# Kernel tuning notes

Hardware: AMD Instinct MI355X
Metric: run time of the kernel (lower is better)

The kernel has to match this reference:

```python
import jax, jax.numpy as jnp
import numpy as np

NEG_INF = -9e15  # same masking constant as the original
LEAKY_ALPHA = 0.2  # tf.nn.leaky_relu default


def setup_inputs() -> dict:
    key = jax.random.key(0)
    k1, k2, k3, k4 = jax.random.split(key, 4)
    N, D, F = 8192, 256, 64
    features = jax.random.normal(k1, (N, D), dtype=jnp.float32)
    adj = jax.random.randint(k2, (N, N), 0, 2, dtype=jnp.int32)
    W = jax.random.normal(k3, (D, F), dtype=jnp.float32) * (1.0 / np.sqrt(D))
    a = jax.random.normal(k4, (2 * F, 1), dtype=jnp.float32) * 0.1
    return {"features": features, "adj": adj, "W": W, "a": a}


def reference(features, adj, W, a):
    # h = X W : [N, F]
    h = features @ W
    F = h.shape[1]
    # a^T [h_i || h_j] = (h a1)_i + (h a2)_j  -- avoids the N*N*2F concat tensor
    a1, a2 = a[:F], a[F:]            # [F,1] each
    e = jax.nn.leaky_relu((h @ a1) + (h @ a2).T, LEAKY_ALPHA)  # [N, N]
    scores = jnp.where(adj > 0, e, jnp.float32(NEG_INF))
    attention = jax.nn.softmax(scores, axis=1)                  # masked softmax over neighbors j
    h_prime = attention @ h                                     # [N, F]
    return jax.nn.elu(h_prime)
```

## Files before the change

### kernel.cpp

```cpp
#include <hip/hip_runtime.h>
#include <hip/hip_bf16.h>
#include <math.h>

#define NN 8192
#define DD 256
#define FF 64
#define NSPLIT 16
#define JCHUNK (NN / NSPLIT)
#define CT 128
#define NT (JCHUNK / CT)

typedef __attribute__((ext_vector_type(8))) short bf16x8;
typedef __attribute__((ext_vector_type(4))) float f32x4;

__device__ __forceinline__ float lrelu(float x) { return fmaxf(x, 0.2f * x); }
__device__ __forceinline__ ushort f2bf(float x) {
  union { __hip_bfloat16 b; ushort s; } u;
  u.b = __float2bfloat16(x);
  return u.s;
}
__device__ __forceinline__ float bf2f(ushort s) {
  union { uint u; float f; } v;
  v.u = (uint)s << 16;
  return v.f;
}

__global__ __launch_bounds__(256) void k_pre(const float* __restrict__ W,
                                             ushort* __restrict__ WT) {
  const int e4 = (blockIdx.x * 256 + threadIdx.x) * 4;
  const float4 wv = *(const float4*)(W + e4);
  const int k = e4 >> 6, d = e4 & 63;
  WT[(d + 0) * DD + k] = f2bf(wv.x);
  WT[(d + 1) * DD + k] = f2bf(wv.y);
  WT[(d + 2) * DD + k] = f2bf(wv.z);
  WT[(d + 3) * DD + k] = f2bf(wv.w);
}

__global__ __launch_bounds__(256) void k_h(
    const float* __restrict__ feat, const ushort* __restrict__ WT,
    const float* __restrict__ a, ushort* __restrict__ hTf,
    float* __restrict__ s1, float* __restrict__ s2) {
  __shared__ float sp1[4][16], sp2[4][16];
  const int t = threadIdx.x, lane = t & 63, w = t >> 6;
  const int il = lane & 15, kg = lane >> 4;
  const int ibase = blockIdx.x * 16;
  const int d = w * 16 + il;
  const float* frow = feat + (size_t)(ibase + il) * DD + kg * 8;
  const ushort* wrow = WT + (size_t)d * DD + kg * 8;
  f32x4 acc = {0.f, 0.f, 0.f, 0.f};
#pragma unroll
  for (int k0 = 0; k0 < DD; k0 += 32) {
    const float4 fa = *(const float4*)(frow + k0);
    const float4 fb = *(const float4*)(frow + k0 + 4);
    bf16x8 av;
    av[0] = f2bf(fa.x); av[1] = f2bf(fa.y); av[2] = f2bf(fa.z); av[3] = f2bf(fa.w);
    av[4] = f2bf(fb.x); av[5] = f2bf(fb.y); av[6] = f2bf(fb.z); av[7] = f2bf(fb.w);
    const bf16x8 bv = *(const bf16x8*)(wrow + k0);
    acc = __builtin_amdgcn_mfma_f32_16x16x32_bf16(av, bv, acc, 0, 0, 0);
  }
  ushort4 hv;
  hv.x = f2bf(acc[0]);
  hv.y = f2bf(acc[1]);
  hv.z = f2bf(acc[2]);
  hv.w = f2bf(acc[3]);
  {
    const int i0q = ibase + kg * 4;
    const size_t hb = ((size_t)(w * 256 + (i0q >> 5)) * 64 +
                       ((i0q >> 3) & 3) * 16 + il) * 8 + (i0q & 7);
    *(ushort4*)(hTf + hb) = hv;
  }
  const float a1v = a[d], a2v = a[FF + d];
#pragma unroll
  for (int r = 0; r < 4; ++r) {
    float v1 = acc[r] * a1v;
    float v2 = acc[r] * a2v;
#pragma unroll
    for (int m = 1; m <= 8; m <<= 1) {
      v1 += __shfl_xor(v1, m);
      v2 += __shfl_xor(v2, m);
    }
    if (il == 0) {
      sp1[w][kg * 4 + r] = v1;
      sp2[w][kg * 4 + r] = v2;
    }
  }
  __syncthreads();
  if (t < 16) {
    s1[ibase + t] = sp1[0][t] + sp1[1][t] + sp1[2][t] + sp1[3][t];
    s2[ibase + t] = sp2[0][t] + sp2[1][t] + sp2[2][t] + sp2[3][t];
  }
}

__global__ __launch_bounds__(256) void k_attn(
    const int* __restrict__ adj, const ushort* __restrict__ hTf,
    const float* __restrict__ s1g, const float* __restrict__ s2g,
    float* __restrict__ pacc, float* __restrict__ pl) {
  __shared__ __align__(16) char smem[4][4480];
  __shared__ float s1w[4][16];
  const int t = threadIdx.x;
  const int lane = t & 63, w = t >> 6;
  const int il = lane & 15, kg = lane >> 4;
  const int ig = blockIdx.x >> 4, js = blockIdx.x & 15;
  const int rbase = ig * 64 + w * 16;
  const int jwin0 = js * JCHUNK;
  char* const smemw = smem[w];

  if (lane < 16) s1w[w][lane] = s1g[rbase + lane];
  const int arow = lane >> 5;
  const int acol = (lane & 31) * 4;
  const int* ap = adj + (size_t)(rbase + arow) * NN + jwin0 + acol;

  float lacc = 0.f;
  f32x4 acc[4] = {{0,0,0,0},{0,0,0,0},{0,0,0,0},{0,0,0,0}};

  for (int tile = 0; tile < NT; ++tile) {
    const int jt = jwin0 + tile * CT;
    const float4 s2v = *(const float4*)(s2g + jt + acol);
#pragma unroll
    for (int rep = 0; rep < 8; ++rep) {
      const int r = rep * 2 + arow;
      const int4 av = *(const int4*)(ap + (size_t)rep * 2 * NN + tile * CT);
      const float s1v = s1w[w][r];
      const float mi = lrelu(s1v + 8.0f);
      ushort4 pk;
      pk.x = av.x ? f2bf(__expf(lrelu(s1v + s2v.x) - mi)) : (ushort)0;
      pk.y = av.y ? f2bf(__expf(lrelu(s1v + s2v.y) - mi)) : (ushort)0;
      pk.z = av.z ? f2bf(__expf(lrelu(s1v + s2v.z) - mi)) : (ushort)0;
      pk.w = av.w ? f2bf(__expf(lrelu(s1v + s2v.w) - mi)) : (ushort)0;
      const int swz = r * 256 + ((acol * 2) ^ ((r & 7) << 4));
      *(ushort4*)(smemw + swz) = pk;
    }
#pragma unroll
    for (int sb = 0; sb < 4; ++sb) {
      const int coff = (sb * 32 + kg * 8) * 2;
      const bf16x8 pb = *(const bf16x8*)(smemw + il * 256 + (coff ^ ((il & 7) << 4)));
      float ps = 0.f;
#pragma unroll
      for (int e = 0; e < 8; ++e) ps += bf2f((ushort)pb[e]);
      lacc += ps;
      const int j32 = (jt >> 5) + sb;
#pragma unroll
      for (int f = 0; f < 4; ++f) {
        const bf16x8 hv =
            *(const bf16x8*)(hTf + ((size_t)(f * 256 + j32) * 64 + lane) * 8);
        acc[f] = __builtin_amdgcn_mfma_f32_16x16x32_bf16(hv, pb, acc[f], 0, 0, 0);
      }
    }
  }
  lacc += __shfl_xor(lacc, 16);
  lacc += __shfl_xor(lacc, 32);
  if (lane < 16) pl[(size_t)js * NN + rbase + lane] = lacc;
  float (*tr)[65] = (float(*)[65])smemw;
#pragma unroll
  for (int f = 0; f < 4; ++f)
#pragma unroll
    for (int r = 0; r < 4; ++r) tr[il][f * 16 + kg * 4 + r] = acc[f][r];
#pragma unroll
  for (int r = 0; r < 16; ++r)
    pacc[((size_t)js * NN + rbase + r) * FF + lane] = tr[r][lane];
}

__global__ __launch_bounds__(256) void k_combine(
    const float* __restrict__ pacc, const float* __restrict__ pl,
    float* __restrict__ out) {
  const int idx = blockIdx.x * 256 + threadIdx.x;
  const int i = idx >> 6;
  float s = 0.f, L = 0.f;
#pragma unroll
  for (int sp = 0; sp < NSPLIT; ++sp) {
    s += pacc[(size_t)sp * NN * FF + idx];
    L += pl[(size_t)sp * NN + i];
  }
  float x = s / fmaxf(L, 1e-30f);
  out[idx] = x > 0.f ? x : expm1f(x);
}

extern "C" void kernel_launch(void* const* d_in, const int* in_sizes, int n_in,
                              void* d_out, int out_size, void* d_ws, size_t ws_size,
                              hipStream_t stream) {
  const float* feat = (const float*)d_in[0];
  const int* adj = (const int*)d_in[1];
  const float* W = (const float*)d_in[2];
  const float* a = (const float*)d_in[3];
  float* out = (float*)d_out;

  ushort* hTf = (ushort*)d_ws;
  ushort* WT = hTf + (size_t)FF * NN;
  float* s1 = (float*)(WT + (size_t)FF * DD);
  float* s2 = s1 + NN;
  float* pl = s2 + NN;
  float* pacc = pl + (size_t)NSPLIT * NN;

  hipLaunchKernelGGL(k_pre, dim3(DD * FF / 1024), dim3(256), 0, stream, W, WT);
  hipLaunchKernelGGL(k_h, dim3(NN / 16), dim3(256), 0, stream, feat, WT, a, hTf, s1, s2);
  hipLaunchKernelGGL(k_attn, dim3((NN / 64) * NSPLIT), dim3(256), 0, stream,
                     adj, hTf, s1, s2, pacc, pl);
  hipLaunchKernelGGL(k_combine, dim3(NN * FF / 256), dim3(256), 0, stream,
                     pacc, pl, out);
}
```

Before: 386.9 us.

## Pack adjacency into a bitmask in a streaming pre-pass and halve the j-split

Adds a grid-stride kernel that reads the int32 adjacency matrix and packs it into a 1-bit-per-entry mask using warp shuffles. The attention kernel then reads compact mask words instead of int4 adjacency loads, so the heavy 256MB read is moved into a simple streaming pass and out of the latency-sensitive MFMA loop. The number of j-splits drops from 16 to 8, which halves the partial-result traffic in the combine step but also halves the attention grid. The cost is an extra kernel launch plus an 8MB mask write and read.

Result: slower. 451.2 us (+16.6%).

```diff
diff --git a/kernel.cpp b/kernel.cpp
--- a/kernel.cpp
+++ b/kernel.cpp
@@ -5,7 +5,7 @@
 #define NN 8192
 #define DD 256
 #define FF 64
-#define NSPLIT 16
+#define NSPLIT 8
 #define JCHUNK (NN / NSPLIT)
 #define CT 128
 #define NT (JCHUNK / CT)
@@ -34,6 +34,22 @@
   WT[(d + 1) * DD + k] = f2bf(wv.y);
   WT[(d + 2) * DD + k] = f2bf(wv.z);
   WT[(d + 3) * DD + k] = f2bf(wv.w);
+}
+
+__global__ __launch_bounds__(256) void k_mask(const int* __restrict__ adj,
+                                              uint* __restrict__ mask) {
+  const size_t nquad = (size_t)NN * NN / 4;
+  const size_t stride = (size_t)gridDim.x * 256;
+  const int lane = threadIdx.x & 63;
+  for (size_t q = (size_t)blockIdx.x * 256 + threadIdx.x; q < nquad; q += stride) {
+    const int4 v = ((const int4*)adj)[q];
+    uint nib = (uint)(v.x & 1) | ((uint)(v.y & 1) << 1) |
+               ((uint)(v.z & 1) << 2) | ((uint)(v.w & 1) << 3);
+    uint b = nib | ((uint)__shfl_xor((int)nib, 1) << 4);
+    b |= (uint)__shfl_xor((int)b, 2) << 8;
+    b |= (uint)__shfl_xor((int)b, 4) << 16;
+    if ((lane & 7) == 0) mask[q >> 3] = b;
+  }
 }
 
 __global__ __launch_bounds__(256) void k_h(
@@ -92,7 +108,7 @@
 }
 
 __global__ __launch_bounds__(256) void k_attn(
-    const int* __restrict__ adj, const ushort* __restrict__ hTf,
+    const uint* __restrict__ mask, const ushort* __restrict__ hTf,
     const float* __restrict__ s1g, const float* __restrict__ s2g,
     float* __restrict__ pacc, float* __restrict__ pl) {
   __shared__ __align__(16) char smem[4][4480];
@@ -100,7 +116,7 @@
   const int t = threadIdx.x;
   const int lane = t & 63, w = t >> 6;
   const int il = lane & 15, kg = lane >> 4;
-  const int ig = blockIdx.x >> 4, js = blockIdx.x & 15;
+  const int ig = blockIdx.x >> 3, js = blockIdx.x & 7;
   const int rbase = ig * 64 + w * 16;
   const int jwin0 = js * JCHUNK;
   char* const smemw = smem[w];
@@ -108,7 +124,9 @@
   if (lane < 16) s1w[w][lane] = s1g[rbase + lane];
   const int arow = lane >> 5;
   const int acol = (lane & 31) * 4;
-  const int* ap = adj + (size_t)(rbase + arow) * NN + jwin0 + acol;
+  const int nsh = (lane & 7) * 4;
+  const uint* mrow = mask + (size_t)(rbase + arow) * (NN / 32) + (jwin0 >> 5) +
+                     ((lane & 31) >> 3);
 
   float lacc = 0.f;
   f32x4 acc[4] = {{0,0,0,0},{0,0,0,0},{0,0,0,0},{0,0,0,0}};
@@ -119,14 +137,15 @@
 #pragma unroll
     for (int rep = 0; rep < 8; ++rep) {
       const int r = rep * 2 + arow;
-      const int4 av = *(const int4*)(ap + (size_t)rep * 2 * NN + tile * CT);
+      const uint mv = mrow[(size_t)(rep * 2) * (NN / 32) + tile * (CT / 32)];
+      const uint nib = (mv >> nsh) & 0xfu;
       const float s1v = s1w[w][r];
       const float mi = lrelu(s1v + 8.0f);
       ushort4 pk;
-      pk.x = av.x ? f2bf(__expf(lrelu(s1v + s2v.x) - mi)) : (ushort)0;
-      pk.y = av.y ? f2bf(__expf(lrelu(s1v + s2v.y) - mi)) : (ushort)0;
-      pk.z = av.z ? f2bf(__expf(lrelu(s1v + s2v.z) - mi)) : (ushort)0;
-      pk.w = av.w ? f2bf(__expf(lrelu(s1v + s2v.w) - mi)) : (ushort)0;
+      pk.x = (nib & 1u) ? f2bf(__expf(lrelu(s1v + s2v.x) - mi)) : (ushort)0;
+      pk.y = (nib & 2u) ? f2bf(__expf(lrelu(s1v + s2v.y) - mi)) : (ushort)0;
+      pk.z = (nib & 4u) ? f2bf(__expf(lrelu(s1v + s2v.z) - mi)) : (ushort)0;
+      pk.w = (nib & 8u) ? f2bf(__expf(lrelu(s1v + s2v.w) - mi)) : (ushort)0;
       const int swz = r * 256 + ((acol * 2) ^ ((r & 7) << 4));
       *(ushort4*)(smemw + swz) = pk;
     }
@@ -141,9 +160,9 @@
       const int j32 = (jt >> 5) + sb;
 #pragma unroll
       for (int f = 0; f < 4; ++f) {
-        const bf16x8 hv =
+        const bf16x8 hvv =
             *(const bf16x8*)(hTf + ((size_t)(f * 256 + j32) * 64 + lane) * 8);
-        acc[f] = __builtin_amdgcn_mfma_f32_16x16x32_bf16(hv, pb, acc[f], 0, 0, 0);
+        acc[f] = __builtin_amdgcn_mfma_f32_16x16x32_bf16(hvv, pb, acc[f], 0, 0, 0);
       }
     }
   }
@@ -190,11 +209,13 @@
   float* s2 = s1 + NN;
   float* pl = s2 + NN;
   float* pacc = pl + (size_t)NSPLIT * NN;
+  uint* mask = (uint*)(pacc + (size_t)NSPLIT * NN * FF);
 
   hipLaunchKernelGGL(k_pre, dim3(DD * FF / 1024), dim3(256), 0, stream, W, WT);
   hipLaunchKernelGGL(k_h, dim3(NN / 16), dim3(256), 0, stream, feat, WT, a, hTf, s1, s2);
+  hipLaunchKernelGGL(k_mask, dim3(2048), dim3(256), 0, stream, adj, mask);
   hipLaunchKernelGGL(k_attn, dim3((NN / 64) * NSPLIT), dim3(256), 0, stream,
-                     adj, hTf, s1, s2, pacc, pl);
+                     mask, hTf, s1, s2, pacc, pl);
   hipLaunchKernelGGL(k_combine, dim3(NN * FF / 256), dim3(256), 0, stream,
                      pacc, pl, out);
 }
```
